# Optimization experiments

Hardware: AMD Instinct MI355X
Metric: run time of the kernel (lower is better)

The kernel has to match this reference:

```python
import jax, jax.numpy as jnp
import numpy as np

HEADS = 8
LANDMARKS = 256
PINV_ITERS = 6
CONV_K = 33


def _layernorm(x, g, b, eps=1e-5):
    mu = x.mean(-1, keepdims=True)
    var = x.var(-1, keepdims=True)
    return (x - mu) * jax.lax.rsqrt(var + eps) * g + b


def _pinv(x, iters=PINV_ITERS):
    # Moore-Penrose iterative pseudo-inverse (lucidrains nystrom-attention)
    ax = jnp.abs(x)
    denom = ax.sum(-1).max() * ax.sum(-2).max()  # global max, as in torch.max()
    z = jnp.swapaxes(x, -1, -2) / denom
    I = jnp.eye(x.shape[-1], dtype=x.dtype)
    for _ in range(iters):
        xz = x @ z
        z = 0.25 * z @ (13 * I - xz @ (15 * I - xz @ (7 * I - xz)))
    return z


def _nystrom_attn(x, qkv_w, out_w, out_b, conv_w):
    b, n, dim = x.shape
    h, m = HEADS, LANDMARKS
    dh = dim // h
    pad = (-n) % m  # pad at the FRONT so n divisible by num_landmarks
    xp = jnp.pad(x, ((0, 0), (pad, 0), (0, 0)))
    npad = n + pad
    qkv = xp @ qkv_w  # [b, npad, 3*dim]
    q, k, v = jnp.split(qkv, 3, axis=-1)

    def to_heads(t):
        return t.reshape(b, npad, h, dh).transpose(0, 2, 1, 3)  # [b,h,npad,dh]

    q, k, v = to_heads(q), to_heads(k), to_heads(v)
    q = q * (dh ** -0.5)
    l = npad // m  # tokens per landmark
    q_l = q.reshape(b, h, m, l, dh).mean(3)  # landmark means [b,h,m,dh]
    k_l = k.reshape(b, h, m, l, dh).mean(3)
    a1 = jax.nn.softmax(jnp.einsum('bhid,bhjd->bhij', q, k_l), axis=-1)   # [b,h,npad,m]
    a2 = jax.nn.softmax(jnp.einsum('bhid,bhjd->bhij', q_l, k_l), axis=-1)  # [b,h,m,m]
    a3 = jax.nn.softmax(jnp.einsum('bhid,bhjd->bhij', q_l, k), axis=-1)   # [b,h,m,npad]
    out = (a1 @ _pinv(a2)) @ (a3 @ v)  # [b,h,npad,dh]
    # residual depthwise conv over sequence dim, one channel per head (bias=False)
    res = jax.lax.conv_general_dilated(
        v, conv_w, window_strides=(1, 1),
        padding=((CONV_K // 2, CONV_K // 2), (0, 0)),
        dimension_numbers=('NCHW', 'OIHW', 'NCHW'),
        feature_group_count=HEADS)
    out = out + res
    out = out.transpose(0, 2, 1, 3).reshape(b, npad, dim)
    out = out @ out_w + out_b
    return out[:, -n:]  # drop front padding


def setup_inputs():
    key = jax.random.key(0)
    ks = jax.random.split(key, 16)
    D_IN, D, C = 1024, 512, 2
    return {
        'feats': jax.random.normal(ks[0], (2, 8000, D_IN), jnp.float32),
        'fc1_w': jax.random.normal(ks[1], (D_IN, D), jnp.float32) * 0.02,
        'fc1_b': jnp.zeros((D,), jnp.float32),
        'cls_token': jax.random.normal(ks[2], (1, 1, D), jnp.float32),
        'ln1_g': jnp.ones((D,), jnp.float32),
        'ln1_b': jnp.zeros((D,), jnp.float32),
        'qkv1_w': jax.random.normal(ks[3], (D, 3 * D), jnp.float32) * 0.02,
        'out1_w': jax.random.normal(ks[4], (D, D), jnp.float32) * 0.02,
        'out1_b': jnp.zeros((D,), jnp.float32),
        'conv1_w': jax.random.normal(ks[5], (HEADS, 1, CONV_K, 1), jnp.float32) * 0.02,
        'ln2_g': jnp.ones((D,), jnp.float32),
        'ln2_b': jnp.zeros((D,), jnp.float32),
        'qkv2_w': jax.random.normal(ks[6], (D, 3 * D), jnp.float32) * 0.02,
        'out2_w': jax.random.normal(ks[7], (D, D), jnp.float32) * 0.02,
        'out2_b': jnp.zeros((D,), jnp.float32),
        'conv2_w': jax.random.normal(ks[8], (HEADS, 1, CONV_K, 1), jnp.float32) * 0.02,
        'normf_g': jnp.ones((D,), jnp.float32),
        'normf_b': jnp.zeros((D,), jnp.float32),
        'fc2_w': jax.random.normal(ks[9], (D, C), jnp.float32) * 0.02,
        'fc2_b': jnp.zeros((C,), jnp.float32),
    }


def reference(feats, fc1_w, fc1_b, cls_token, ln1_g, ln1_b, qkv1_w, out1_w, out1_b, conv1_w,
              ln2_g, ln2_b, qkv2_w, out2_w, out2_b, conv2_w, normf_g, normf_b, fc2_w, fc2_b):
    h = jax.nn.relu(feats @ fc1_w + fc1_b)  # [B,N,512]
    B = h.shape[0]
    cls = jnp.broadcast_to(cls_token, (B, 1, cls_token.shape[-1]))
    h = jnp.concatenate([cls, h], axis=1)  # [B,N+1,512]
    h = h + _nystrom_attn(_layernorm(h, ln1_g, ln1_b), qkv1_w, out1_w, out1_b, conv1_w)
    h = h + _nystrom_attn(_layernorm(h, ln2_g, ln2_b), qkv2_w, out2_w, out2_b, conv2_w)
    h_cls = _layernorm(h, normf_g, normf_b)[:, 0]
    logits = h_cls @ fc2_w + fc2_b
    y_prob = jax.nn.softmax(logits, axis=1)
    y_hat = jnp.argmax(logits, axis=1)
    return logits, y_prob, y_hat
```

## Files before the change

### kernel.cpp

```cpp
#include <hip/hip_runtime.h>

typedef unsigned short u16;
typedef __attribute__((ext_vector_type(8))) short short8;
typedef __attribute__((ext_vector_type(4))) float f32x4;

__device__ __forceinline__ float bf2f(u16 x){
  union { unsigned u; float f; } c; c.u = ((unsigned)x) << 16; return c.f;
}
__device__ __forceinline__ u16 f2bf(float f){
  union { float f; unsigned u; } c; c.f = f;
  unsigned u = c.u;
  return (u16)((u + 0x7FFFu + ((u >> 16) & 1u)) >> 16);
}
__device__ __forceinline__ unsigned pk2(float a, float b){
  return (unsigned)f2bf(a) | ((unsigned)f2bf(b) << 16);
}
__device__ __forceinline__ void hilo(float v, u16& hi, u16& lo){
  hi = f2bf(v); lo = f2bf(v - bf2f(hi));
}

__device__ __forceinline__ void gload16(const void* g, void* l){
  __builtin_amdgcn_global_load_lds(
    (const __attribute__((address_space(1))) void*)g,
    (__attribute__((address_space(3))) void*)l, 16, 0, 0);
}

__global__ void k_cls(const float* cls, float* h){
  int b = blockIdx.x, t = threadIdx.x;
  for (int c=t; c<512; c+=256)
    h[((long)b*8192+191)*512 + c] = cls[c];
}

__global__ void k_cvtT(const float* Wm, u16* wT, int K, int N){
  __shared__ float tile[32][33];
  int n0 = blockIdx.x*32, k0 = blockIdx.y*32;
  int x = threadIdx.x & 31, y = threadIdx.x >> 5;
  #pragma unroll
  for (int p=0;p<4;p++) tile[y+8*p][x] = Wm[(long)(k0+y+8*p)*N + n0 + x];
  __syncthreads();
  #pragma unroll
  for (int p=0;p<4;p++) wT[(long)(n0+y+8*p)*K + k0 + x] = f2bf(tile[x][y+8*p]);
}

template<int MODE>
__launch_bounds__(256)
__global__ void k_gemm(const void* Av, const u16* Bt, const float* bias,
                       float* hout, float* qo, float* ko, float* vo,
                       int M, int N, int K){
  __shared__ __align__(16) u16 As[128*32];
  __shared__ __align__(16) u16 Bs[128*32];
  const int tid = threadIdx.x;
  const int wave = tid>>6, lane = tid&63;
  const int m0 = blockIdx.x*128, n0 = blockIdx.y*128;
  const int wr = wave>>1, wc = wave&1;
  f32x4 acc[4][4];
  #pragma unroll
  for (int i=0;i<4;i++)
    #pragma unroll
    for (int j=0;j<4;j++) acc[i][j] = (f32x4){0.f,0.f,0.f,0.f};

  for (int k0=0; k0<K; k0+=32){
    if constexpr (MODE == 0){
      int r = tid>>1, half = tid&1;
      const float* gp = (const float*)Av + (long)(m0+r)*K + k0 + half*16;
      float4 f0 = *(const float4*)(gp+0);
      float4 f1 = *(const float4*)(gp+4);
      float4 f2 = *(const float4*)(gp+8);
      float4 f3 = *(const float4*)(gp+12);
      uint4 pa, pb;
      pa.x = pk2(f0.x,f0.y); pa.y = pk2(f0.z,f0.w);
      pa.z = pk2(f1.x,f1.y); pa.w = pk2(f1.z,f1.w);
      pb.x = pk2(f2.x,f2.y); pb.y = pk2(f2.z,f2.w);
      pb.z = pk2(f3.x,f3.y); pb.w = pk2(f3.z,f3.w);
      uint4* dst = (uint4*)&As[r*32 + half*16];
      dst[0] = pa; dst[1] = pb;
    } else {
      #pragma unroll
      for (int ci=0; ci<2; ++ci){
        int c = wave*2 + ci;
        int r = (c<<4) + (lane>>2), kq = lane&3;
        const u16* gp;
        if constexpr (MODE == 1){
          gp = (const u16*)Av + (long)(m0+r)*K + k0 + kq*8;
        } else {
          int rr = m0 + r; int b = rr>>13, pos = rr&8191;
          int cc = k0 + kq*8; int hh = cc>>6, d = cc&63;
          gp = (const u16*)Av + ((long)(b*8+hh)*8192 + pos)*64 + d;
        }
        gload16(gp, &As[c*512]);
      }
    }
    #pragma unroll
    for (int ci=0; ci<2; ++ci){
      int c = wave*2 + ci;
      int r = (c<<4) + (lane>>2), kq = lane&3;
      gload16(Bt + (long)(n0+r)*K + k0 + kq*8, &Bs[c*512]);
    }
    __syncthreads();
    short8 af[4], bf[4];
    int arow = wr*64 + (lane&15);
    int brow = wc*64 + (lane&15);
    int koff = (lane>>4)*8;
    #pragma unroll
    for (int i=0;i<4;i++){
      af[i] = *(const short8*)&As[(arow + i*16)*32 + koff];
      bf[i] = *(const short8*)&Bs[(brow + i*16)*32 + koff];
    }
    #pragma unroll
    for (int i=0;i<4;i++)
      #pragma unroll
      for (int j=0;j<4;j++)
        acc[i][j] = __builtin_amdgcn_mfma_f32_16x16x32_bf16(bf[j], af[i], acc[i][j], 0,0,0);
    __syncthreads();
  }

  const int lc = lane&15, hi4 = (lane>>4)*4;
  if constexpr (MODE == 0){
    #pragma unroll
    for (int j=0;j<4;j++){
      int cb = n0 + wc*64 + j*16 + hi4;
      float4 bb = *(const float4*)&bias[cb];
      #pragma unroll
      for (int i=0;i<4;i++){
        int row = m0 + wr*64 + i*16 + lc;
        int b = (row >= 8000) ? 1 : 0;
        int tok = row - b*8000;
        float4 o;
        o.x = fmaxf(acc[i][j][0] + bb.x, 0.f);
        o.y = fmaxf(acc[i][j][1] + bb.y, 0.f);
        o.z = fmaxf(acc[i][j][2] + bb.z, 0.f);
        o.w = fmaxf(acc[i][j][3] + bb.w, 0.f);
        *(float4*)&hout[((long)(b*8192 + 192 + tok))*512 + cb] = o;
      }
    }
  } else if constexpr (MODE == 1){
    #pragma unroll
    for (int j=0;j<4;j++){
      int cb = n0 + wc*64 + j*16 + hi4;
      int which = cb>>9, head = (cb>>6)&7, d = cb&63;
      float* base = (which==0) ? qo : (which==1 ? ko : vo);
      float scale = (which==0) ? 0.125f : 1.0f;
      #pragma unroll
      for (int i=0;i<4;i++){
        int row = m0 + wr*64 + i*16 + lc;
        int b = row>>13, pos = row&8191;
        float4 o;
        o.x = acc[i][j][0]*scale; o.y = acc[i][j][1]*scale;
        o.z = acc[i][j][2]*scale; o.w = acc[i][j][3]*scale;
        *(float4*)&base[((long)(b*8+head)*8192 + pos)*64 + d] = o;
      }
    }
  } else {
    #pragma unroll
    for (int j=0;j<4;j++){
      int cb = n0 + wc*64 + j*16 + hi4;
      float4 bb = *(const float4*)&bias[cb];
      #pragma unroll
      for (int i=0;i<4;i++){
        int row = m0 + wr*64 + i*16 + lc;
        int pos = row&8191;
        if (pos < 191) continue;
        float4* p = (float4*)&hout[(long)row*512 + cb];
        float4 cur = *p;
        cur.x += acc[i][j][0] + bb.x;
        cur.y += acc[i][j][1] + bb.y;
        cur.z += acc[i][j][2] + bb.z;
        cur.w += acc[i][j][3] + bb.w;
        *p = cur;
      }
    }
  }
}

__global__ void k_ln(const float* hsrc, const float* g, const float* bt, u16* xlnb){
  int row = blockIdx.x;
  int pos = row & 8191;
  int t = threadIdx.x;
  long base = (long)row*512 + t*2;
  if (pos < 191){ *(unsigned*)&xlnb[base] = 0u; return; }
  float2 x = *(const float2*)(hsrc + base);
  __shared__ float red[4];
  float s = x.x + x.y;
  for (int off=32; off; off>>=1) s += __shfl_down(s, off, 64);
  if ((t&63)==0) red[t>>6]=s;
  __syncthreads();
  float mean = (red[0]+red[1]+red[2]+red[3]) * (1.f/512.f);
  __syncthreads();
  float d0 = x.x-mean, d1 = x.y-mean;
  float ss = d0*d0 + d1*d1;
  for (int off=32; off; off>>=1) ss += __shfl_down(ss, off, 64);
  if ((t&63)==0) red[t>>6]=ss;
  __syncthreads();
  float rstd = rsqrtf((red[0]+red[1]+red[2]+red[3])*(1.f/512.f) + 1e-5f);
  float o0 = d0*rstd*g[t*2]   + bt[t*2];
  float o1 = d1*rstd*g[t*2+1] + bt[t*2+1];
  *(unsigned*)&xlnb[base] = pk2(o0, o1);
}

__global__ void k_landmark(const float* src, float* dst){
  int g = blockIdx.x, bh = blockIdx.y, d = threadIdx.x;
  const float* p = src + (((long)bh*8192) + g*32)*64 + d;
  float s = 0.f;
  #pragma unroll
  for (int j=0;j<32;j++) s += p[j*64];
  dst[((long)bh*256 + g)*64 + d] = s*(1.f/32.f);
}

__launch_bounds__(256)
__global__ void k_a2(const float* qlm, const float* klm, float* a2, u16* a2Nh, u16* a2Nl){
  __shared__ float qls[16][68];
  __shared__ float kls[64][65];
  __shared__ float Sf[16][260];
  __shared__ float red[4];
  int bh = blockIdx.y, rt = blockIdx.x, t = threadIdx.x;
  const float* qp = qlm + ((long)bh*256 + rt*16)*64;
  { int fidx = t*4; int r = fidx>>6, c = fidx&63;
    float4 a = *(const float4*)(qp + fidx);
    qls[r][c]=a.x; qls[r][c+1]=a.y; qls[r][c+2]=a.z; qls[r][c+3]=a.w; }
  const float* kp = klm + (long)bh*16384;
  int cl = t & 63, ig = t >> 6;
  for (int kt=0; kt<4; ++kt){
    __syncthreads();
    for (int l=0;l<4;l++){
      int fidx = (l*256+t)*4; int r = fidx>>6, c = fidx&63;
      float4 a = *(const float4*)(kp + (long)(kt*64+r)*64 + c);
      kls[r][c]=a.x; kls[r][c+1]=a.y; kls[r][c+2]=a.z; kls[r][c+3]=a.w;
    }
    __syncthreads();
    float s0=0,s1=0,s2=0,s3=0;
    #pragma unroll
    for (int d=0;d<64;d++){
      float kv = kls[cl][d];
      s0 += qls[ig*4+0][d]*kv;
      s1 += qls[ig*4+1][d]*kv;
      s2 += qls[ig*4+2][d]*kv;
      s3 += qls[ig*4+3][d]*kv;
    }
    Sf[ig*4+0][kt*64+cl]=s0;
    Sf[ig*4+1][kt*64+cl]=s1;
    Sf[ig*4+2][kt*64+cl]=s2;
    Sf[ig*4+3][kt*64+cl]=s3;
  }
  __syncthreads();
  long ab = ((long)bh*256 + rt*16)*256;
  for (int i=0;i<16;i++){
    float val = Sf[i][t];
    float m = val;
    for (int off=1; off<64; off<<=1) m = fmaxf(m, __shfl_xor(m,off,64));
    if ((t&63)==0) red[t>>6]=m;
    __syncthreads();
    m = fmaxf(fmaxf(red[0],red[1]),fmaxf(red[2],red[3]));
    __syncthreads();
    float e = __expf(val - m);
    float sum = e;
    for (int off=1; off<64; off<<=1) sum += __shfl_xor(sum,off,64);
    if ((t&63)==0) red[t>>6]=sum;
    __syncthreads();
    sum = red[0]+red[1]+red[2]+red[3];
    __syncthreads();
    float o = e/sum;
    long idx = ab + (long)i*256 + t;
    a2[idx] = o;
    u16 hi, lo; hilo(o, hi, lo);
    a2Nh[idx]=hi; a2Nl[idx]=lo;
  }
}

__global__ void k_colrow(const float* a2, float* rc){
  int bh = blockIdx.x, t = threadIdx.x;
  const float* p = a2 + (long)bh*65536;
  float cs=0.f, rs=0.f;
  for (int r=0;r<256;r++) cs += fabsf(p[(long)r*256 + t]);
  for (int c=0;c<256;c++) rs += fabsf(p[(long)t*256 + c]);
  __shared__ float red[4];
  for (int off=32; off; off>>=1) cs = fmaxf(cs, __shfl_down(cs,off,64));
  if ((t&63)==0) red[t>>6]=cs;
  __syncthreads();
  if (t==0) rc[bh] = fmaxf(fmaxf(red[0],red[1]),fmaxf(red[2],red[3]));
  __syncthreads();
  for (int off=32; off; off>>=1) rs = fmaxf(rs, __shfl_down(rs,off,64));
  if ((t&63)==0) red[t>>6]=rs;
  __syncthreads();
  if (t==0) rc[16+bh] = fmaxf(fmaxf(red[0],red[1]),fmaxf(red[2],red[3]));
}
__global__ void k_denom(const float* rc, float* denom){
  float cm=0.f, rm=0.f;
  for (int i=0;i<16;i++){ cm=fmaxf(cm,rc[i]); rm=fmaxf(rm,rc[16+i]); }
  *denom = cm*rm;
}

__global__ void k_z0p(const float* a2, const float* denom,
                      u16* zNh, u16* zNl, u16* zTh, u16* zTl){
  __shared__ float tile[32][33];
  int bh = blockIdx.z;
  int c0 = blockIdx.x*32, r0 = blockIdx.y*32;
  int x = threadIdx.x & 31, y = threadIdx.x >> 5;
  const float* p = a2 + (long)bh*65536;
  float inv = 1.0f / (*denom);
  long zb = (long)bh*65536;
  #pragma unroll
  for (int yy=0; yy<32; yy+=8){
    float vv = p[(long)(r0+y+yy)*256 + c0 + x];
    tile[y+yy][x] = vv;
    float val = vv*inv;
    u16 hi, lo; hilo(val, hi, lo);
    long idx = zb + (long)(r0+y+yy)*256 + c0 + x;
    zTh[idx]=hi; zTl[idx]=lo;
  }
  __syncthreads();
  #pragma unroll
  for (int yy=0; yy<32; yy+=8){
    float val = tile[x][y+yy]*inv;
    u16 hi, lo; hilo(val, hi, lo);
    long idx = zb + (long)(c0+y+yy)*256 + r0 + x;
    zNh[idx]=hi; zNl[idx]=lo;
  }
}

struct NC {
  const u16 *Ah, *Al, *Bh, *Bl;
  const u16 *E1h, *E1l, *E2h, *E2l;
  u16 *oNh, *oNl, *oTh, *oTl, *oBF;
  long strA, strB, strO;
  float sa, s1, s2;
};

__launch_bounds__(256)
__global__ void k_nmm(NC c0, NC c1){
  int gz = blockIdx.z;
  int bh = gz & 15;
  NC C = (gz>>4) ? c1 : c0;
  __shared__ __align__(16) char smem[64*68*4];
  u16* AsH = (u16*)smem;
  u16* AsL = (u16*)(smem + 4096);
  u16* BsH = (u16*)(smem + 8192);
  u16* BsL = (u16*)(smem + 12288);
  float* T = (float*)smem;
  int tid = threadIdx.x, wave = tid>>6, lane = tid&63;
  int m0 = blockIdx.x*64, n0 = blockIdx.y*64;
  int wr = wave>>1, wc = wave&1;
  int lc = lane&15, hi = lane>>4;
  f32x4 acc[2][2];
  #pragma unroll
  for (int i=0;i<2;i++)
    #pragma unroll
    for (int j=0;j<2;j++) acc[i][j] = (f32x4){0.f,0.f,0.f,0.f};

  const u16* plane = (wave==0) ? C.Ah : (wave==1) ? C.Al : (wave==2) ? C.Bh : C.Bl;
  long pstr = (wave<2) ? C.strA : C.strB;
  int rbase = (wave<2) ? m0 : n0;
  const u16* pb = plane + (long)bh*pstr;
  char* dstbase = smem + wave*4096;
  int srow = lane>>2, skq = lane&3;

  for (int k0=0; k0<256; k0+=32){
    #pragma unroll
    for (int ii=0; ii<4; ++ii){
      int row = ii*16 + srow;
      int kcs = k0 + ((skq ^ ((row>>1)&3))<<3);
      gload16(pb + (long)(rbase+row)*256 + kcs, dstbase + ii*1024);
    }
    __syncthreads();
    short8 aH[2], aL[2], bH[2], bL[2];
    #pragma unroll
    for (int i=0;i<2;i++){
      int ra = wr*32 + i*16 + lc;
      int ca = ((hi ^ ((ra>>1)&3)))*8;
      aH[i] = *(const short8*)&AsH[ra*32 + ca];
      aL[i] = *(const short8*)&AsL[ra*32 + ca];
      int rb = wc*32 + i*16 + lc;
      int cb = ((hi ^ ((rb>>1)&3)))*8;
      bH[i] = *(const short8*)&BsH[rb*32 + cb];
      bL[i] = *(const short8*)&BsL[rb*32 + cb];
    }
    #pragma unroll
    for (int i=0;i<2;i++)
      #pragma unroll
      for (int j=0;j<2;j++){
        acc[i][j] = __builtin_amdgcn_mfma_f32_16x16x32_bf16(aH[i], bH[j], acc[i][j], 0,0,0);
        acc[i][j] = __builtin_amdgcn_mfma_f32_16x16x32_bf16(aH[i], bL[j], acc[i][j], 0,0,0);
        acc[i][j] = __builtin_amdgcn_mfma_f32_16x16x32_bf16(aL[i], bH[j], acc[i][j], 0,0,0);
      }
    __syncthreads();
  }

  long eb = (long)bh*65536;
  #pragma unroll
  for (int i=0;i<2;i++)
    #pragma unroll
    for (int j=0;j<2;j++){
      int rg = wr*32 + i*16 + hi*4;
      int cg = wc*32 + j*16 + lc;
      #pragma unroll
      for (int r=0;r<4;r++){
        float val = C.sa*acc[i][j][r];
        long ei = eb + (long)(m0+rg+r)*256 + (n0+cg);
        if (C.E1h) val += C.s1*(bf2f(C.E1h[ei]) + bf2f(C.E1l[ei]));
        if (C.E2h) val += C.s2*(bf2f(C.E2h[ei]) + bf2f(C.E2l[ei]));
        T[(rg+r)*68 + cg] = val;
      }
    }
  __syncthreads();
  int rr = tid>>2, cc0 = (tid&3)*16;
  if (C.oBF){
    u16 tmp[16];
    #pragma unroll
    for (int m=0;m<16;m++) tmp[m] = f2bf(T[rr*68 + cc0 + m]);
    long ob = (long)bh*C.strO + (long)(m0+rr)*256 + n0 + cc0;
    *(uint4*)&C.oBF[ob] = *(uint4*)&tmp[0];
    *(uint4*)&C.oBF[ob+8] = *(uint4*)&tmp[8];
  } else {
    u16 th[16], tl[16];
    #pragma unroll
    for (int m=0;m<16;m++) hilo(T[rr*68 + cc0 + m], th[m], tl[m]);
    long ob = (long)bh*65536 + (long)(m0+rr)*256 + n0 + cc0;
    *(uint4*)&C.oNh[ob]   = *(uint4*)&th[0];
    *(uint4*)&C.oNh[ob+8] = *(uint4*)&th[8];
    *(uint4*)&C.oNl[ob]   = *(uint4*)&tl[0];
    *(uint4*)&C.oNl[ob+8] = *(uint4*)&tl[8];
    if (C.oTh){
      #pragma unroll
      for (int m=0;m<16;m++) hilo(T[(cc0+m)*68 + rr], th[m], tl[m]);
      long obt = (long)bh*65536 + (long)(n0+rr)*256 + m0 + cc0;
      *(uint4*)&C.oTh[obt]   = *(uint4*)&th[0];
      *(uint4*)&C.oTh[obt+8] = *(uint4*)&th[8];
      *(uint4*)&C.oTl[obt]   = *(uint4*)&tl[0];
      *(uint4*)&C.oTl[obt+8] = *(uint4*)&tl[8];
    }
  }
}

__launch_bounds__(256)
__global__ void k_vt(const float* v, u16* vt){
  __shared__ float tile[32][68];
  int pt = blockIdx.x, bh = blockIdx.y, t = threadIdx.x;
  int p = t>>3, d0 = (t&7)*8;
  const float* src = v + ((long)bh*8192 + pt*32 + p)*64 + d0;
  float4 a = *(const float4*)src;
  float4 b = *(const float4*)(src+4);
  tile[p][d0+0]=a.x; tile[p][d0+1]=a.y; tile[p][d0+2]=a.z; tile[p][d0+3]=a.w;
  tile[p][d0+4]=b.x; tile[p][d0+5]=b.y; tile[p][d0+6]=b.z; tile[p][d0+7]=b.w;
  __syncthreads();
  int pos2 = (t&15)*2;
  #pragma unroll
  for (int ll=0; ll<4; ++ll){
    int d = (t>>4) + 16*ll;
    unsigned val = pk2(tile[pos2][d], tile[pos2+1][d]);
    *(unsigned*)&vt[((long)(bh*64 + d))*8192 + pt*32 + pos2] = val;
  }
}

template<int OM>
__launch_bounds__(256)
__global__ void k_flash2(const float* Q, const float* K, const u16* VT,
                         float* op, float* ml, u16* hb,
                         int kvchunk, long qbh, long kbh, long vtbh, int vtrow){
  __shared__ __align__(16) u16 KT[64*64];
  __shared__ __align__(16) u16 VTs[64*64];
  __shared__ __align__(16) u16 Pb[4*16*72];
  int bh = blockIdx.y, qt = blockIdx.x, sk = (OM==0) ? blockIdx.z : 0;
  int t = threadIdx.x, w = t>>6, l = t&63;
  int lq = l&15, hi = l>>4;

  short8 qf[2];
  {
    const float* qp = Q + (long)bh*qbh + (long)(qt*64 + w*16 + lq)*64 + hi*8;
    #pragma unroll
    for (int kh=0; kh<2; ++kh){
      float4 f0 = *(const float4*)(qp + kh*32);
      float4 f1 = *(const float4*)(qp + kh*32 + 4);
      union { short8 s; uint4 u; } c;
      c.u.x = pk2(f0.x,f0.y); c.u.y = pk2(f0.z,f0.w);
      c.u.z = pk2(f1.x,f1.y); c.u.w = pk2(f1.z,f1.w);
      qf[kh] = c.s;
    }
  }
  float m_run = -1e30f, l_run = 0.f;
  f32x4 o[4];
  #pragma unroll
  for (int i=0;i<4;i++) o[i] = (f32x4){0.f,0.f,0.f,0.f};

  const float* kbase = K + (long)bh*kbh;
  const u16* vtbase = VT + (long)bh*vtbh;
  char* Pw = (char*)&Pb[w*16*72];
  int kv0 = sk*kvchunk;

  for (int p0 = kv0; p0 < kv0 + kvchunk; p0 += 64){
    {
      int r = w*16 + (l>>2), d0 = (l&3)*16;
      const float* kr = kbase + (long)(p0 + r)*64 + d0;
      float4 f0 = *(const float4*)(kr+0);
      float4 f1 = *(const float4*)(kr+4);
      float4 f2 = *(const float4*)(kr+8);
      float4 f3 = *(const float4*)(kr+12);
      float fv[16] = {f0.x,f0.y,f0.z,f0.w,f1.x,f1.y,f1.z,f1.w,
                      f2.x,f2.y,f2.z,f2.w,f3.x,f3.y,f3.z,f3.w};
      #pragma unroll
      for (int m=0;m<8;m++){
        int d = d0 + 2*m;
        int byte = (r*128 + d*2) ^ ((r&7)<<4);
        *(unsigned*)((char*)KT + byte) = pk2(fv[2*m], fv[2*m+1]);
      }
    }
    #pragma unroll
    for (int ii=0; ii<2; ++ii){
      int inst = w*2 + ii;
      int d = inst*8 + (l>>3);
      int srcoff = ((l&7)*16) ^ ((d&7)<<4);
      const char* src = (const char*)(vtbase + (long)d*vtrow + p0) + srcoff;
      gload16(src, (char*)VTs + inst*1024);
    }
    __syncthreads();
    f32x4 s[4];
    #pragma unroll
    for (int i=0;i<4;i++){
      s[i] = (f32x4){0.f,0.f,0.f,0.f};
      #pragma unroll
      for (int kh=0;kh<2;kh++){
        int kvr = i*16 + lq;
        int byte = (kvr*128 + hi*16 + kh*64) ^ ((kvr&7)<<4);
        short8 kf = *(const short8*)((const char*)KT + byte);
        s[i] = __builtin_amdgcn_mfma_f32_16x16x32_bf16(kf, qf[kh], s[i], 0,0,0);
      }
    }
    float tm = -1e30f;
    #pragma unroll
    for (int i=0;i<4;i++)
      #pragma unroll
      for (int r=0;r<4;r++) tm = fmaxf(tm, s[i][r]);
    tm = fmaxf(tm, __shfl_xor(tm, 16));
    tm = fmaxf(tm, __shfl_xor(tm, 32));
    float mnew = fmaxf(m_run, tm);
    float scale = __expf(m_run - mnew);
    float tsum = 0.f;
    #pragma unroll
    for (int i=0;i<4;i++)
      #pragma unroll
      for (int r=0;r<4;r++){ float e = __expf(s[i][r]-mnew); s[i][r]=e; tsum += e; }
    tsum += __shfl_xor(tsum, 16);
    tsum += __shfl_xor(tsum, 32);
    l_run = l_run*scale + tsum;
    m_run = mnew;
    #pragma unroll
    for (int i=0;i<4;i++)
      #pragma unroll
      for (int r=0;r<4;r++) o[i][r] *= scale;
    #pragma unroll
    for (int i=0;i<4;i++){
      int byte = lq*144 + (i*16 + hi*4)*2;
      *(unsigned*)(Pw + byte)     = pk2(s[i][0], s[i][1]);
      *(unsigned*)(Pw + byte + 4) = pk2(s[i][2], s[i][3]);
    }
    short8 pf[2];
    #pragma unroll
    for (int kh=0;kh<2;kh++)
      pf[kh] = *(const short8*)(Pw + lq*144 + hi*16 + kh*64);
    #pragma unroll
    for (int i=0;i<4;i++){
      #pragma unroll
      for (int kh=0;kh<2;kh++){
        int d = i*16 + lq;
        int byte = (d*128 + hi*16 + kh*64) ^ ((d&7)<<4);
        short8 vf = *(const short8*)((const char*)VTs + byte);
        o[i] = __builtin_amdgcn_mfma_f32_16x16x32_bf16(vf, pf[kh], o[i], 0,0,0);
      }
    }
    __syncthreads();
  }

  int qrow = qt*64 + w*16 + lq;
  if constexpr (OM == 0){
    long ob = ((long)(sk*16+bh)*256 + qrow)*64;
    #pragma unroll
    for (int i=0;i<4;i++)
      #pragma unroll
      for (int r=0;r<4;r++) op[ob + i*16 + hi*4 + r] = o[i][r];
    if (l < 16){
      long mi = ((long)(sk*16+bh)*256 + qt*64 + w*16 + l)*2;
      ml[mi] = m_run; ml[mi+1] = l_run;
    }
  } else {
    float invl = 1.f/l_run;
    long hb0 = ((long)bh*8192 + qrow)*64;
    #pragma unroll
    for (int i=0;i<4;i++)
      #pragma unroll
      for (int r=0;r<4;r++){
        long idx = hb0 + i*16 + hi*4 + r;
        hb[idx] = f2bf(bf2f(hb[idx]) + o[i][r]*invl);
      }
  }
}

__global__ void k_fcomb(const float* op, const float* ml, u16* w3Th, u16* w3Tl){
  int bh = blockIdx.y, rt = blockIdx.x, t = threadIdx.x;
  int row = rt*16 + (t>>4), d0 = (t&15)*4;
  float M = -1e30f;
  for (int s=0;s<16;s++) M = fmaxf(M, ml[(((long)(s*16+bh)*256)+row)*2]);
  float lt = 0.f;
  float4 o = {0,0,0,0};
  for (int s=0;s<16;s++){
    long base = ((long)(s*16+bh)*256)+row;
    float w = __expf(ml[base*2]-M);
    lt += ml[base*2+1]*w;
    float4 ov = *(const float4*)&op[base*64 + d0];
    o.x += ov.x*w; o.y += ov.y*w; o.z += ov.z*w; o.w += ov.w*w;
  }
  float inv = 1.f/lt;
  float vals[4] = {o.x*inv, o.y*inv, o.z*inv, o.w*inv};
  #pragma unroll
  for (int dd=0; dd<4; ++dd){
    u16 hi, lo; hilo(vals[dd], hi, lo);
    long idx = (long)bh*32768 + (long)(d0+dd)*256 + row;
    w3Th[idx]=hi; w3Tl[idx]=lo;
  }
}

__launch_bounds__(256)
__global__ void k_conv(const float* v, const float* cw, u16* heads){
  __shared__ float vsl[160][64];
  __shared__ float cws[33];
  int bh = blockIdx.y, pt = blockIdx.x, t = threadIdx.x;
  int hh = bh & 7;
  if (t < 33) cws[t] = cw[hh*33 + t];
  int p0 = pt*128;
  const float* vp = v + (long)bh*8192*64;
  for (int l=0;l<10;l++){
    int fidx = (l*256 + t)*4;
    int r = fidx>>6, c = fidx&63;
    int gp = p0 - 16 + r;
    if (gp>=0 && gp<8192){
      float4 a = *(const float4*)(vp + (long)gp*64 + c);
      vsl[r][c]=a.x; vsl[r][c+1]=a.y; vsl[r][c+2]=a.z; vsl[r][c+3]=a.w;
    } else {
      vsl[r][c]=0.f; vsl[r][c+1]=0.f; vsl[r][c+2]=0.f; vsl[r][c+3]=0.f;
    }
  }
  __syncthreads();
  int d = t & 63, pg = t >> 6;
  u16* hp = heads + ((long)bh*8192 + p0)*64;
  for (int pp=0; pp<32; pp++){
    int pl = pp*4 + pg;
    float acc = 0.f;
    #pragma unroll
    for (int tt=0; tt<33; tt++) acc += vsl[pl+tt][d]*cws[tt];
    hp[(long)pl*64 + d] = f2bf(acc);
  }
}

__global__ void k_final(const float* hbuf, const float* g, const float* bt,
                        const float* fw, const float* fb, float* outp){
  int b = blockIdx.x, t = threadIdx.x;
  __shared__ float red[4];
  __shared__ float sx[512];
  __shared__ float lg[4];
  const float* x = hbuf + ((long)b*8192+191)*512;
  float2 xv = *(const float2*)(x + t*2);
  float s = xv.x + xv.y;
  for (int off=32; off; off>>=1) s += __shfl_down(s,off,64);
  if ((t&63)==0) red[t>>6]=s;
  __syncthreads();
  float mean = (red[0]+red[1]+red[2]+red[3])*(1.f/512.f);
  __syncthreads();
  float d0 = xv.x-mean, d1 = xv.y-mean;
  float ssq = d0*d0 + d1*d1;
  for (int off=32; off; off>>=1) ssq += __shfl_down(ssq,off,64);
  if ((t&63)==0) red[t>>6]=ssq;
  __syncthreads();
  float rstd = rsqrtf((red[0]+red[1]+red[2]+red[3])*(1.f/512.f) + 1e-5f);
  sx[t*2]   = d0*rstd*g[t*2]   + bt[t*2];
  sx[t*2+1] = d1*rstd*g[t*2+1] + bt[t*2+1];
  __syncthreads();
  int c = t>>7, jj = t&127;
  float part = 0.f;
  for (int kk=jj; kk<512; kk+=128) part += sx[kk]*fw[(long)kk*2 + c];
  for (int off=1; off<64; off<<=1) part += __shfl_xor(part,off,64);
  if ((t&63)==0) lg[t>>6]=part;
  __syncthreads();
  if (t==0){
    float l0 = lg[0]+lg[1] + fb[0];
    float l1 = lg[2]+lg[3] + fb[1];
    float m = fmaxf(l0,l1);
    float e0 = __expf(l0-m), e1 = __expf(l1-m);
    float inv = 1.f/(e0+e1);
    outp[b*2+0]=l0; outp[b*2+1]=l1;
    outp[4+b*2+0]=e0*inv; outp[4+b*2+1]=e1*inv;
    outp[8+b]=(l1>l0) ? 1.f : 0.f;
  }
}

static NC mkc(const u16* Ah,const u16* Al,const u16* Bh,const u16* Bl,
              const u16* E1h,const u16* E1l,const u16* E2h,const u16* E2l,
              u16* oNh,u16* oNl,u16* oTh,u16* oTl,u16* oBF,
              long strA,long strB,long strO,float sa,float s1,float s2){
  NC c; c.Ah=Ah;c.Al=Al;c.Bh=Bh;c.Bl=Bl;c.E1h=E1h;c.E1l=E1l;c.E2h=E2h;c.E2l=E2l;
  c.oNh=oNh;c.oNl=oNl;c.oTh=oTh;c.oTl=oTl;c.oBF=oBF;
  c.strA=strA;c.strB=strB;c.strO=strO;c.sa=sa;c.s1=s1;c.s2=s2; return c;
}

extern "C" void kernel_launch(void* const* d_in, const int* in_sizes, int n_in,
                              void* d_out, int out_size, void* d_ws, size_t ws_size,
                              hipStream_t stream){
  (void)in_sizes; (void)n_in; (void)out_size; (void)ws_size;
  const long TOK = (long)2*8192*512;
  const long PL = 1048576;
  float* W    = (float*)d_ws;
  float* rc   = W;
  float* h    = W + 64;
  float* q    = h + TOK;
  float* k    = q + TOK;
  float* v    = k + TOK;
  u16*  xlnb  = (u16*)(v + TOK);
  u16*  zPl   = xlnb;
  u16*  headsb= xlnb + TOK;
  u16*  wT    = headsb + TOK;
  float* ql   = (float*)(wT + PL);
  float* kl   = ql + 262144;
  float* a2f  = kl + 262144;
  u16*  a2Nh  = (u16*)(a2f + 1048576);
  u16*  a2Nl  = a2Nh + PL;
  u16*  YNh   = a2Nl + PL;
  u16*  YNl   = YNh + PL;
  u16*  YTh   = YNl + PL;
  u16*  YTl   = YTh + PL;
  u16*  Gth   = YTl + PL;
  u16*  Gtl   = Gth + PL;
  u16*  PNh   = Gtl + PL;
  u16*  PNl   = PNh + PL;
  u16*  PTh   = PNl + PL;
  u16*  PTl   = PTh + PL;
  u16*  w3Th  = PTl + PL;
  u16*  w3Tl  = w3Th + 524288;
  u16*  zwT   = w3Tl + 524288;
  u16*  vt    = zwT + 262144;
  float* op   = v;
  float* ml   = a2f;

  u16* zN_h[2] = { zPl,        zPl + 4*PL };
  u16* zN_l[2] = { zPl + PL,   zPl + 5*PL };
  u16* zT_h[2] = { zPl + 2*PL, zPl + 6*PL };
  u16* zT_l[2] = { zPl + 3*PL, zPl + 7*PL };

  dim3 B(256);

  k_cls<<<dim3(2), B, 0, stream>>>((const float*)d_in[3], h);
  k_cvtT<<<dim3(16,32), B, 0, stream>>>((const float*)d_in[1], wT, 1024, 512);
  k_gemm<0><<<dim3(125,4), B, 0, stream>>>(d_in[0], wT, (const float*)d_in[2],
                                           h, nullptr,nullptr,nullptr, 16000,512,1024);

  for (int blk=0; blk<2; ++blk){
    const float* lng  = (const float*)d_in[blk?10:4];
    const float* lnb  = (const float*)d_in[blk?11:5];
    const float* qkvw = (const float*)d_in[blk?12:6];
    const float* outw = (const float*)d_in[blk?13:7];
    const float* outb = (const float*)d_in[blk?14:8];
    const float* cw   = (const float*)d_in[blk?15:9];

    k_ln<<<dim3(16384), B, 0, stream>>>(h, lng, lnb, xlnb);

    k_cvtT<<<dim3(48,16), B, 0, stream>>>(qkvw, wT, 512, 1536);
    k_gemm<1><<<dim3(128,12), B, 0, stream>>>(xlnb, wT, nullptr,
                                              nullptr, q,k,v, 16384,1536,512);

    k_landmark<<<dim3(256,16), dim3(64), 0, stream>>>(q, ql);
    k_landmark<<<dim3(256,16), dim3(64), 0, stream>>>(k, kl);

    k_vt<<<dim3(256,16), B, 0, stream>>>(v, vt);
    k_conv<<<dim3(64,16), B, 0, stream>>>(v, cw, headsb);

    k_a2<<<dim3(16,16), B, 0, stream>>>(ql, kl, a2f, a2Nh, a2Nl);
    k_colrow<<<dim3(16), B, 0, stream>>>(a2f, rc);
    k_denom<<<dim3(1), dim3(1), 0, stream>>>(rc, rc+32);
    k_z0p<<<dim3(8,8,16), B, 0, stream>>>(a2f, rc+32, zN_h[0],zN_l[0],zT_h[0],zT_l[0]);

    for (int it=0; it<6; ++it){
      int zi = it&1, zo = (it+1)&1;
      NC s1 = mkc(a2Nh,a2Nl, zT_h[zi],zT_l[zi], nullptr,nullptr,nullptr,nullptr,
                  YNh,YNl, YTh,YTl, nullptr, 65536,65536,0, 1.f,0.f,0.f);
      k_nmm<<<dim3(4,4,16), B, 0, stream>>>(s1, s1);
      NC s2a = mkc(YTh,YTl, YNh,YNl, YTh,YTl, nullptr,nullptr,
                   Gth,Gtl, nullptr,nullptr, nullptr, 65536,65536,0, -1.f,7.f,0.f);
      NC s2b = mkc(zN_h[zi],zN_l[zi], YTh,YTl, nullptr,nullptr,nullptr,nullptr,
                   PNh,PNl, PTh,PTl, nullptr, 65536,65536,0, 1.f,0.f,0.f);
      k_nmm<<<dim3(4,4,32), B, 0, stream>>>(s2a, s2b);
      NC s3 = mkc(PNh,PNl, Gth,Gtl, zN_h[zi],zN_l[zi], PNh,PNl,
                  zN_h[zo],zN_l[zo], zT_h[zo],zT_l[zo], nullptr,
                  65536,65536,0, 0.25f,3.25f,-3.75f);
      k_nmm<<<dim3(4,4,16), B, 0, stream>>>(s3, s3);
    }

    k_flash2<0><<<dim3(4,16,16), B, 0, stream>>>(ql, k, vt, op, ml, nullptr,
                                                 512, 16384L, 524288L, 524288L, 8192);
    k_fcomb<<<dim3(16,16), B, 0, stream>>>(op, ml, w3Th, w3Tl);
    NC zwc = mkc(w3Th,w3Tl, zN_h[0],zN_l[0], nullptr,nullptr,nullptr,nullptr,
                 nullptr,nullptr,nullptr,nullptr, zwT, 32768,65536,16384, 1.f,0.f,0.f);
    k_nmm<<<dim3(1,4,16), B, 0, stream>>>(zwc, zwc);
    k_flash2<1><<<dim3(128,16,1), B, 0, stream>>>(q, kl, zwT, nullptr, nullptr, headsb,
                                                  256, 524288L, 16384L, 16384L, 256);

    k_cvtT<<<dim3(16,16), B, 0, stream>>>(outw, wT, 512, 512);
    k_gemm<2><<<dim3(128,4), B, 0, stream>>>(headsb, wT, outb,
                                             h, nullptr,nullptr,nullptr, 16384,512,512);
  }

  k_final<<<dim3(2), B, 0, stream>>>(h, (const float*)d_in[16], (const float*)d_in[17],
                                     (const float*)d_in[18], (const float*)d_in[19], (float*)d_out);
}
```

Measured before the change: 1.202 ms.

## Store Q/K/V in bf16, use async K loads, shrink nmm tiles to 32x32

The QKV GEMM now writes bf16 q/k/v instead of fp32, and landmark, transpose, conv and flash kernels read bf16 directly. The flash kernel loads K tiles with global_load_lds instead of converting fp32 in registers. Landmark means are also stored as bf16 copies. Separately, the iterative pinv matmul kernel drops to single-wave 32x32 tiles with four times as many blocks, to raise parallelism on these small 256x256 products. This roughly halves q/k/v memory traffic, at the cost of bf16 rounding of q, k and v before the conv and landmark means.

```diff
diff --git a/kernel.cpp b/kernel.cpp
--- a/kernel.cpp
+++ b/kernel.cpp
@@ -45,7 +45,7 @@
 template<int MODE>
 __launch_bounds__(256)
 __global__ void k_gemm(const void* Av, const u16* Bt, const float* bias,
-                       float* hout, float* qo, float* ko, float* vo,
+                       float* hout, u16* qo, u16* ko, u16* vo,
                        int M, int N, int K){
   __shared__ __align__(16) u16 As[128*32];
   __shared__ __align__(16) u16 Bs[128*32];
@@ -138,16 +138,16 @@
     for (int j=0;j<4;j++){
       int cb = n0 + wc*64 + j*16 + hi4;
       int which = cb>>9, head = (cb>>6)&7, d = cb&63;
-      float* base = (which==0) ? qo : (which==1 ? ko : vo);
+      u16* base = (which==0) ? qo : (which==1 ? ko : vo);
       float scale = (which==0) ? 0.125f : 1.0f;
       #pragma unroll
       for (int i=0;i<4;i++){
         int row = m0 + wr*64 + i*16 + lc;
         int b = row>>13, pos = row&8191;
-        float4 o;
-        o.x = acc[i][j][0]*scale; o.y = acc[i][j][1]*scale;
-        o.z = acc[i][j][2]*scale; o.w = acc[i][j][3]*scale;
-        *(float4*)&base[((long)(b*8+head)*8192 + pos)*64 + d] = o;
+        unsigned o2[2];
+        o2[0] = pk2(acc[i][j][0]*scale, acc[i][j][1]*scale);
+        o2[1] = pk2(acc[i][j][2]*scale, acc[i][j][3]*scale);
+        *(uint2*)&base[((long)(b*8+head)*8192 + pos)*64 + d] = *(uint2*)o2;
       }
     }
   } else {
@@ -197,13 +197,16 @@
   *(unsigned*)&xlnb[base] = pk2(o0, o1);
 }
 
-__global__ void k_landmark(const float* src, float* dst){
+__global__ void k_landmark(const u16* src, float* dst, u16* dstb){
   int g = blockIdx.x, bh = blockIdx.y, d = threadIdx.x;
-  const float* p = src + (((long)bh*8192) + g*32)*64 + d;
+  const u16* p = src + (((long)bh*8192) + g*32)*64 + d;
   float s = 0.f;
   #pragma unroll
-  for (int j=0;j<32;j++) s += p[j*64];
-  dst[((long)bh*256 + g)*64 + d] = s*(1.f/32.f);
+  for (int j=0;j<32;j++) s += bf2f(p[j*64]);
+  s *= (1.f/32.f);
+  long o = ((long)bh*256 + g)*64 + d;
+  dst[o] = s;
+  dstb[o] = f2bf(s);
 }
 
 __launch_bounds__(256)
@@ -325,20 +328,19 @@
   float sa, s1, s2;
 };
 
-__launch_bounds__(256)
+__launch_bounds__(64)
 __global__ void k_nmm(NC c0, NC c1){
   int gz = blockIdx.z;
   int bh = gz & 15;
   NC C = (gz>>4) ? c1 : c0;
-  __shared__ __align__(16) char smem[64*68*4];
+  __shared__ __align__(16) char smem[8192];
   u16* AsH = (u16*)smem;
-  u16* AsL = (u16*)(smem + 4096);
-  u16* BsH = (u16*)(smem + 8192);
-  u16* BsL = (u16*)(smem + 12288);
+  u16* AsL = (u16*)(smem + 2048);
+  u16* BsH = (u16*)(smem + 4096);
+  u16* BsL = (u16*)(smem + 6144);
   float* T = (float*)smem;
-  int tid = threadIdx.x, wave = tid>>6, lane = tid&63;
-  int m0 = blockIdx.x*64, n0 = blockIdx.y*64;
-  int wr = wave>>1, wc = wave&1;
+  int lane = threadIdx.x;
+  int m0 = blockIdx.x*32, n0 = blockIdx.y*32;
   int lc = lane&15, hi = lane>>4;
   f32x4 acc[2][2];
   #pragma unroll
@@ -346,32 +348,36 @@
     #pragma unroll
     for (int j=0;j<2;j++) acc[i][j] = (f32x4){0.f,0.f,0.f,0.f};
 
-  const u16* plane = (wave==0) ? C.Ah : (wave==1) ? C.Al : (wave==2) ? C.Bh : C.Bl;
-  long pstr = (wave<2) ? C.strA : C.strB;
-  int rbase = (wave<2) ? m0 : n0;
-  const u16* pb = plane + (long)bh*pstr;
-  char* dstbase = smem + wave*4096;
-  int srow = lane>>2, skq = lane&3;
+  const u16* pAh = C.Ah + (long)bh*C.strA;
+  const u16* pAl = C.Al + (long)bh*C.strA;
+  const u16* pBh = C.Bh + (long)bh*C.strB;
+  const u16* pBl = C.Bl + (long)bh*C.strB;
+  int r0 = lane>>2, kq = lane&3;
+  int r1 = r0 + 16;
+  long offA0 = (long)(m0+r0)*256 + ((kq ^ ((r0>>1)&3))<<3);
+  long offA1 = (long)(m0+r1)*256 + ((kq ^ ((r1>>1)&3))<<3);
+  long offB0 = (long)(n0+r0)*256 + ((kq ^ ((r0>>1)&3))<<3);
+  long offB1 = (long)(n0+r1)*256 + ((kq ^ ((r1>>1)&3))<<3);
 
   for (int k0=0; k0<256; k0+=32){
-    #pragma unroll
-    for (int ii=0; ii<4; ++ii){
-      int row = ii*16 + srow;
-      int kcs = k0 + ((skq ^ ((row>>1)&3))<<3);
-      gload16(pb + (long)(rbase+row)*256 + kcs, dstbase + ii*1024);
-    }
+    gload16(pAh + offA0 + k0, smem + 0);
+    gload16(pAh + offA1 + k0, smem + 1024);
+    gload16(pAl + offA0 + k0, smem + 2048);
+    gload16(pAl + offA1 + k0, smem + 3072);
+    gload16(pBh + offB0 + k0, smem + 4096);
+    gload16(pBh + offB1 + k0, smem + 5120);
+    gload16(pBl + offB0 + k0, smem + 6144);
+    gload16(pBl + offB1 + k0, smem + 7168);
     __syncthreads();
     short8 aH[2], aL[2], bH[2], bL[2];
     #pragma unroll
     for (int i=0;i<2;i++){
-      int ra = wr*32 + i*16 + lc;
-      int ca = ((hi ^ ((ra>>1)&3)))*8;
+      int ra = i*16 + lc;
+      int ca = ((hi ^ ((ra>>1)&3)))<<3;
       aH[i] = *(const short8*)&AsH[ra*32 + ca];
       aL[i] = *(const short8*)&AsL[ra*32 + ca];
-      int rb = wc*32 + i*16 + lc;
-      int cb = ((hi ^ ((rb>>1)&3)))*8;
-      bH[i] = *(const short8*)&BsH[rb*32 + cb];
-      bL[i] = *(const short8*)&BsL[rb*32 + cb];
+      bH[i] = *(const short8*)&BsH[ra*32 + ca];
+      bL[i] = *(const short8*)&BsL[ra*32 + ca];
     }
     #pragma unroll
     for (int i=0;i<2;i++)
@@ -389,30 +395,30 @@
   for (int i=0;i<2;i++)
     #pragma unroll
     for (int j=0;j<2;j++){
-      int rg = wr*32 + i*16 + hi*4;
-      int cg = wc*32 + j*16 + lc;
+      int rg = i*16 + hi*4;
+      int cg = j*16 + lc;
       #pragma unroll
       for (int r=0;r<4;r++){
         float val = C.sa*acc[i][j][r];
         long ei = eb + (long)(m0+rg+r)*256 + (n0+cg);
         if (C.E1h) val += C.s1*(bf2f(C.E1h[ei]) + bf2f(C.E1l[ei]));
         if (C.E2h) val += C.s2*(bf2f(C.E2h[ei]) + bf2f(C.E2l[ei]));
-        T[(rg+r)*68 + cg] = val;
-      }
-    }
-  __syncthreads();
-  int rr = tid>>2, cc0 = (tid&3)*16;
+        T[(rg+r)*34 + cg] = val;
+      }
+    }
+  __syncthreads();
+  int rr = lane>>1, cc0 = (lane&1)*16;
   if (C.oBF){
     u16 tmp[16];
     #pragma unroll
-    for (int m=0;m<16;m++) tmp[m] = f2bf(T[rr*68 + cc0 + m]);
+    for (int m=0;m<16;m++) tmp[m] = f2bf(T[rr*34 + cc0 + m]);
     long ob = (long)bh*C.strO + (long)(m0+rr)*256 + n0 + cc0;
-    *(uint4*)&C.oBF[ob] = *(uint4*)&tmp[0];
+    *(uint4*)&C.oBF[ob]   = *(uint4*)&tmp[0];
     *(uint4*)&C.oBF[ob+8] = *(uint4*)&tmp[8];
   } else {
     u16 th[16], tl[16];
     #pragma unroll
-    for (int m=0;m<16;m++) hilo(T[rr*68 + cc0 + m], th[m], tl[m]);
+    for (int m=0;m<16;m++) hilo(T[rr*34 + cc0 + m], th[m], tl[m]);
     long ob = (long)bh*65536 + (long)(m0+rr)*256 + n0 + cc0;
     *(uint4*)&C.oNh[ob]   = *(uint4*)&th[0];
     *(uint4*)&C.oNh[ob+8] = *(uint4*)&th[8];
@@ -420,7 +426,7 @@
     *(uint4*)&C.oNl[ob+8] = *(uint4*)&tl[8];
     if (C.oTh){
       #pragma unroll
-      for (int m=0;m<16;m++) hilo(T[(cc0+m)*68 + rr], th[m], tl[m]);
+      for (int m=0;m<16;m++) hilo(T[(cc0+m)*34 + rr], th[m], tl[m]);
       long obt = (long)bh*65536 + (long)(n0+rr)*256 + m0 + cc0;
       *(uint4*)&C.oTh[obt]   = *(uint4*)&th[0];
       *(uint4*)&C.oTh[obt+8] = *(uint4*)&th[8];
@@ -431,28 +437,22 @@
 }
 
 __launch_bounds__(256)
-__global__ void k_vt(const float* v, u16* vt){
-  __shared__ float tile[32][68];
+__global__ void k_vt(const u16* v, u16* vt){
+  __shared__ u16 tile[32][80];
   int pt = blockIdx.x, bh = blockIdx.y, t = threadIdx.x;
   int p = t>>3, d0 = (t&7)*8;
-  const float* src = v + ((long)bh*8192 + pt*32 + p)*64 + d0;
-  float4 a = *(const float4*)src;
-  float4 b = *(const float4*)(src+4);
-  tile[p][d0+0]=a.x; tile[p][d0+1]=a.y; tile[p][d0+2]=a.z; tile[p][d0+3]=a.w;
-  tile[p][d0+4]=b.x; tile[p][d0+5]=b.y; tile[p][d0+6]=b.z; tile[p][d0+7]=b.w;
-  __syncthreads();
-  int pos2 = (t&15)*2;
-  #pragma unroll
-  for (int ll=0; ll<4; ++ll){
-    int d = (t>>4) + 16*ll;
-    unsigned val = pk2(tile[pos2][d], tile[pos2+1][d]);
-    *(unsigned*)&vt[((long)(bh*64 + d))*8192 + pt*32 + pos2] = val;
-  }
+  *(uint4*)&tile[p][d0] = *(const uint4*)(v + ((long)bh*8192 + pt*32 + p)*64 + d0);
+  __syncthreads();
+  int d = t>>2, seg = t&3;
+  u16 tmp[8];
+  #pragma unroll
+  for (int j=0;j<8;j++) tmp[j] = tile[seg*8+j][d];
+  *(uint4*)&vt[((long)(bh*64 + d))*8192 + pt*32 + seg*8] = *(uint4*)tmp;
 }
 
 template<int OM>
 __launch_bounds__(256)
-__global__ void k_flash2(const float* Q, const float* K, const u16* VT,
+__global__ void k_flash2(const u16* Q, const u16* K, const u16* VT,
                          float* op, float* ml, u16* hb,
                          int kvchunk, long qbh, long kbh, long vtbh, int vtrow){
   __shared__ __align__(16) u16 KT[64*64];
@@ -464,43 +464,27 @@
 
   short8 qf[2];
   {
-    const float* qp = Q + (long)bh*qbh + (long)(qt*64 + w*16 + lq)*64 + hi*8;
-    #pragma unroll
-    for (int kh=0; kh<2; ++kh){
-      float4 f0 = *(const float4*)(qp + kh*32);
-      float4 f1 = *(const float4*)(qp + kh*32 + 4);
-      union { short8 s; uint4 u; } c;
-      c.u.x = pk2(f0.x,f0.y); c.u.y = pk2(f0.z,f0.w);
-      c.u.z = pk2(f1.x,f1.y); c.u.w = pk2(f1.z,f1.w);
-      qf[kh] = c.s;
-    }
+    const u16* qp = Q + (long)bh*qbh + (long)(qt*64 + w*16 + lq)*64 + hi*8;
+    qf[0] = *(const short8*)(qp);
+    qf[1] = *(const short8*)(qp + 32);
   }
   float m_run = -1e30f, l_run = 0.f;
   f32x4 o[4];
   #pragma unroll
   for (int i=0;i<4;i++) o[i] = (f32x4){0.f,0.f,0.f,0.f};
 
-  const float* kbase = K + (long)bh*kbh;
+  const u16* kbase = K + (long)bh*kbh;
   const u16* vtbase = VT + (long)bh*vtbh;
   char* Pw = (char*)&Pb[w*16*72];
   int kv0 = sk*kvchunk;
 
   for (int p0 = kv0; p0 < kv0 + kvchunk; p0 += 64){
-    {
-      int r = w*16 + (l>>2), d0 = (l&3)*16;
-      const float* kr = kbase + (long)(p0 + r)*64 + d0;
-      float4 f0 = *(const float4*)(kr+0);
-      float4 f1 = *(const float4*)(kr+4);
-      float4 f2 = *(const float4*)(kr+8);
-      float4 f3 = *(const float4*)(kr+12);
-      float fv[16] = {f0.x,f0.y,f0.z,f0.w,f1.x,f1.y,f1.z,f1.w,
-                      f2.x,f2.y,f2.z,f2.w,f3.x,f3.y,f3.z,f3.w};
-      #pragma unroll
-      for (int m=0;m<8;m++){
-        int d = d0 + 2*m;
-        int byte = (r*128 + d*2) ^ ((r&7)<<4);
-        *(unsigned*)((char*)KT + byte) = pk2(fv[2*m], fv[2*m+1]);
-      }
+    #pragma unroll
+    for (int ii=0; ii<2; ++ii){
+      int inst = w*2 + ii;
+      int r = inst*8 + (l>>3);
+      int ch = l&7;
+      gload16(kbase + (long)(p0+r)*64 + ((ch ^ (r&7))<<3), (char*)KT + inst*1024);
     }
     #pragma unroll
     for (int ii=0; ii<2; ++ii){
@@ -617,23 +601,26 @@
 }
 
 __launch_bounds__(256)
-__global__ void k_conv(const float* v, const float* cw, u16* heads){
+__global__ void k_conv(const u16* v, const float* cw, u16* heads){
   __shared__ float vsl[160][64];
   __shared__ float cws[33];
   int bh = blockIdx.y, pt = blockIdx.x, t = threadIdx.x;
   int hh = bh & 7;
   if (t < 33) cws[t] = cw[hh*33 + t];
   int p0 = pt*128;
-  const float* vp = v + (long)bh*8192*64;
-  for (int l=0;l<10;l++){
-    int fidx = (l*256 + t)*4;
+  const u16* vp = v + (long)bh*8192*64;
+  for (int l=0;l<5;l++){
+    int fidx = (l*256 + t)*8;
     int r = fidx>>6, c = fidx&63;
     int gp = p0 - 16 + r;
     if (gp>=0 && gp<8192){
-      float4 a = *(const float4*)(vp + (long)gp*64 + c);
-      vsl[r][c]=a.x; vsl[r][c+1]=a.y; vsl[r][c+2]=a.z; vsl[r][c+3]=a.w;
+      uint4 a = *(const uint4*)(vp + (long)gp*64 + c);
+      const u16* pp = (const u16*)&a;
+      #pragma unroll
+      for (int m=0;m<8;m++) vsl[r][c+m] = bf2f(pp[m]);
     } else {
-      vsl[r][c]=0.f; vsl[r][c+1]=0.f; vsl[r][c+2]=0.f; vsl[r][c+3]=0.f;
+      #pragma unroll
+      for (int m=0;m<8;m++) vsl[r][c+m] = 0.f;
     }
   }
   __syncthreads();
@@ -707,16 +694,18 @@
   float* W    = (float*)d_ws;
   float* rc   = W;
   float* h    = W + 64;
-  float* q    = h + TOK;
-  float* k    = q + TOK;
-  float* v    = k + TOK;
-  u16*  xlnb  = (u16*)(v + TOK);
+  u16*  q     = (u16*)(h + TOK);
+  u16*  k     = q + TOK;
+  u16*  v     = k + TOK;
+  u16*  xlnb  = v + TOK;
   u16*  zPl   = xlnb;
   u16*  headsb= xlnb + TOK;
   u16*  wT    = headsb + TOK;
   float* ql   = (float*)(wT + PL);
   float* kl   = ql + 262144;
-  float* a2f  = kl + 262144;
+  u16*  qlb   = (u16*)(kl + 262144);
+  u16*  klb   = qlb + 262144;
+  float* a2f  = (float*)(klb + 262144);
   u16*  a2Nh  = (u16*)(a2f + 1048576);
   u16*  a2Nl  = a2Nh + PL;
   u16*  YNh   = a2Nl + PL;
@@ -733,7 +722,7 @@
   u16*  w3Tl  = w3Th + 524288;
   u16*  zwT   = w3Tl + 524288;
   u16*  vt    = zwT + 262144;
-  float* op   = v;
+  float* op   = (float*)v;
   float* ml   = a2f;
 
   u16* zN_h[2] = { zPl,        zPl + 4*PL };
@@ -762,8 +751,8 @@
     k_gemm<1><<<dim3(128,12), B, 0, stream>>>(xlnb, wT, nullptr,
                                               nullptr, q,k,v, 16384,1536,512);
 
-    k_landmark<<<dim3(256,16), dim3(64), 0, stream>>>(q, ql);
-    k_landmark<<<dim3(256,16), dim3(64), 0, stream>>>(k, kl);
+    k_landmark<<<dim3(256,16), dim3(64), 0, stream>>>(q, ql, qlb);
+    k_landmark<<<dim3(256,16), dim3(64), 0, stream>>>(k, kl, klb);
 
     k_vt<<<dim3(256,16), B, 0, stream>>>(v, vt);
     k_conv<<<dim3(64,16), B, 0, stream>>>(v, cw, headsb);
@@ -777,25 +766,25 @@
       int zi = it&1, zo = (it+1)&1;
       NC s1 = mkc(a2Nh,a2Nl, zT_h[zi],zT_l[zi], nullptr,nullptr,nullptr,nullptr,
                   YNh,YNl, YTh,YTl, nullptr, 65536,65536,0, 1.f,0.f,0.f);
-      k_nmm<<<dim3(4,4,16), B, 0, stream>>>(s1, s1);
+      k_nmm<<<dim3(8,8,16), dim3(64), 0, stream>>>(s1, s1);
       NC s2a = mkc(YTh,YTl, YNh,YNl, YTh,YTl, nullptr,nullptr,
                    Gth,Gtl, nullptr,nullptr, nullptr, 65536,65536,0, -1.f,7.f,0.f);
       NC s2b = mkc(zN_h[zi],zN_l[zi], YTh,YTl, nullptr,nullptr,nullptr,nullptr,
                    PNh,PNl, PTh,PTl, nullptr, 65536,65536,0, 1.f,0.f,0.f);
-      k_nmm<<<dim3(4,4,32), B, 0, stream>>>(s2a, s2b);
+      k_nmm<<<dim3(8,8,32), dim3(64), 0, stream>>>(s2a, s2b);
       NC s3 = mkc(PNh,PNl, Gth,Gtl, zN_h[zi],zN_l[zi], PNh,PNl,
                   zN_h[zo],zN_l[zo], zT_h[zo],zT_l[zo], nullptr,
                   65536,65536,0, 0.25f,3.25f,-3.75f);
-      k_nmm<<<dim3(4,4,16), B, 0, stream>>>(s3, s3);
-    }
-
-    k_flash2<0><<<dim3(4,16,16), B, 0, stream>>>(ql, k, vt, op, ml, nullptr,
+      k_nmm<<<dim3(8,8,16), dim3(64), 0, stream>>>(s3, s3);
+    }
+
+    k_flash2<0><<<dim3(4,16,16), B, 0, stream>>>(qlb, k, vt, op, ml, nullptr,
                                                  512, 16384L, 524288L, 524288L, 8192);
     k_fcomb<<<dim3(16,16), B, 0, stream>>>(op, ml, w3Th, w3Tl);
     NC zwc = mkc(w3Th,w3Tl, zN_h[0],zN_l[0], nullptr,nullptr,nullptr,nullptr,
                  nullptr,nullptr,nullptr,nullptr, zwT, 32768,65536,16384, 1.f,0.f,0.f);
-    k_nmm<<<dim3(1,4,16), B, 0, stream>>>(zwc, zwc);
-    k_flash2<1><<<dim3(128,16,1), B, 0, stream>>>(q, kl, zwT, nullptr, nullptr, headsb,
+    k_nmm<<<dim3(2,8,16), dim3(64), 0, stream>>>(zwc, zwc);
+    k_flash2<1><<<dim3(128,16,1), B, 0, stream>>>(q, klb, zwT, nullptr, nullptr, headsb,
                                                   256, 524288L, 16384L, 16384L, 256);
 
     k_cvtT<<<dim3(16,16), B, 0, stream>>>(outw, wT, 512, 512);
```

Result: no change. 1.205 ms (+0.2%).
